# Performance work log

Measured on AMD Instinct MI355X. Metric: run time of the kernel, lower is better.

The kernel has to match this reference:

```python
import jax, jax.numpy as jnp
import numpy as np

# --- constants mirroring init_kwargs ---
DIM = 1024
N_HEADS = 16
N_KV_HEADS = 4
HEAD_DIM = DIM // N_HEADS          # 64
REP = N_HEADS // N_KV_HEADS        # 4
ROPE_THETA = 10000.0
WINDOW = 512
N_GLOBAL = 64
EPS = 1e-6


def setup_inputs() -> dict:
    key = jax.random.key(0)
    ks = jax.random.split(key, 7)
    B, L = 2, 2048
    x = jax.random.normal(ks[0], (B, L, DIM), dtype=jnp.float32)
    s = 0.02
    wq = jax.random.normal(ks[1], (DIM, N_HEADS * HEAD_DIM), dtype=jnp.float32) * s
    wk = jax.random.normal(ks[2], (DIM, N_KV_HEADS * HEAD_DIM), dtype=jnp.float32) * s
    wv = jax.random.normal(ks[3], (DIM, N_KV_HEADS * HEAD_DIM), dtype=jnp.float32) * s
    wo = jax.random.normal(ks[4], (N_HEADS * HEAD_DIM, DIM), dtype=jnp.float32) * s
    gq = jnp.ones((HEAD_DIM,), dtype=jnp.float32) + 0.01 * jax.random.normal(ks[5], (HEAD_DIM,), dtype=jnp.float32)
    gk = jnp.ones((HEAD_DIM,), dtype=jnp.float32) + 0.01 * jax.random.normal(ks[6], (HEAD_DIM,), dtype=jnp.float32)
    return {"x": x, "wq": wq, "wk": wk, "wv": wv, "wo": wo, "gq": gq, "gk": gk}


def _rmsnorm(t, g):
    # QKNorm: RMS norm over head_dim with learnable per-dim scale
    return t * jax.lax.rsqrt(jnp.mean(t * t, axis=-1, keepdims=True) + EPS) * g


def _rope(t, cos, sin):
    # t: [B,H,L,hd]; complex RoPE over consecutive pairs (2i, 2i+1)
    t1 = t[..., 0::2]
    t2 = t[..., 1::2]
    o1 = t1 * cos - t2 * sin
    o2 = t1 * sin + t2 * cos
    return jnp.stack([o1, o2], axis=-1).reshape(t.shape)


def reference(x, wq, wk, wv, wo, gq, gk):
    B, L, D = x.shape
    q = (x @ wq).reshape(B, L, N_HEADS, HEAD_DIM)
    k = (x @ wk).reshape(B, L, N_KV_HEADS, HEAD_DIM)
    v = (x @ wv).reshape(B, L, N_KV_HEADS, HEAD_DIM)
    q = _rmsnorm(q, gq)
    k = _rmsnorm(k, gk)
    q = q.transpose(0, 2, 1, 3)  # [B,H,L,hd]
    k = k.transpose(0, 2, 1, 3)
    v = v.transpose(0, 2, 1, 3)

    # RoPE frequencies (start_pos = 0)
    inv_freq = 1.0 / (ROPE_THETA ** (jnp.arange(0, HEAD_DIM, 2, dtype=jnp.float32) / HEAD_DIM))
    ang = jnp.arange(L, dtype=jnp.float32)[:, None] * inv_freq[None, :]  # [L, hd/2]
    cos, sin = jnp.cos(ang), jnp.sin(ang)
    q = _rope(q, cos, sin)
    k = _rope(k, cos, sin)

    # GQA: repeat kv heads (repeat_interleave on head dim)
    k = jnp.repeat(k, REP, axis=1)
    v = jnp.repeat(v, REP, axis=1)

    scores = jnp.einsum("bhqd,bhkd->bhqk", q, k) / np.sqrt(HEAD_DIM).astype(np.float32)

    # sliding-window + global-token causal mask
    half = WINDOW // 2
    i = jnp.arange(L)[:, None]
    j = jnp.arange(L)[None, :]
    m = (j <= i) & ((j >= i - half) | (j < N_GLOBAL))  # [L,L] bool
    scores = jnp.where(m[None, None], scores, -jnp.inf)

    attn = jax.nn.softmax(scores.astype(jnp.float32), axis=-1).astype(scores.dtype)
    out = jnp.einsum("bhqk,bhkd->bhqd", attn, v)
    out = out.transpose(0, 2, 1, 3).reshape(B, L, N_HEADS * HEAD_DIM)
    return out @ wo
```

## Files before the change

### kernel.cpp

```cpp
#include <hip/hip_runtime.h>
#include <hip/hip_bf16.h>

typedef __bf16 bf16x8 __attribute__((ext_vector_type(8)));
typedef __bf16 bf16x4 __attribute__((ext_vector_type(4)));
typedef float  f32x4  __attribute__((ext_vector_type(4)));
typedef short  s16x4  __attribute__((ext_vector_type(4)));

__device__ __forceinline__ __bf16 to_bf16(float f) {
    __hip_bfloat16 h = __float2bfloat16(f);
    return *reinterpret_cast<__bf16*>(&h);
}

__device__ __forceinline__ f32x4 mfma32(bf16x8 a, bf16x8 b, f32x4 c) {
    return __builtin_amdgcn_mfma_f32_16x16x32_bf16(a, b, c, 0, 0, 0);
}
__device__ __forceinline__ f32x4 mfma16(bf16x4 a, bf16x4 b, f32x4 c) {
#if __has_builtin(__builtin_amdgcn_mfma_f32_16x16x16_bf16)
    return __builtin_amdgcn_mfma_f32_16x16x16_bf16(a, b, c, 0, 0, 0);
#else
    return __builtin_amdgcn_mfma_f32_16x16x16bf16_1k(
        __builtin_bit_cast(s16x4, a), __builtin_bit_cast(s16x4, b), c, 0, 0, 0);
#endif
}

__device__ __forceinline__ void gload_lds16(const __bf16* g, __bf16* l) {
    __builtin_amdgcn_global_load_lds(
        (const __attribute__((address_space(1))) void*)g,
        (__attribute__((address_space(3))) void*)l, 16, 0, 0);
}


__global__ __launch_bounds__(256) void prep_k(const float* __restrict__ wq,
                                              const float* __restrict__ wk,
                                              const float* __restrict__ wv,
                                              const float* __restrict__ x,
                                              __bf16* __restrict__ WqkvT,
                                              __bf16* __restrict__ xb,
                                              float2* __restrict__ rope_tab) {
    int b = blockIdx.x, tid = threadIdx.x;
    if (b >= 3584) {
        int idx = (b - 3584) * 256 + tid;
        int pos = idx >> 5, f = idx & 31;
        float ex = (float)(2 * f) * (1.0f / 64.0f);
        float invf = expf(-ex * 9.210340371976184f);
        float ang = (float)pos * invf;
        rope_tab[idx] = make_float2(cosf(ang), sinf(ang));
        return;
    }
    if (b >= 1536) {
        int i = ((b - 1536) * 256 + tid) * 8;
        f32x4 a = *(const f32x4*)(x + i);
        f32x4 c = *(const f32x4*)(x + i + 4);
        bf16x8 h;
        h[0] = to_bf16(a.x); h[1] = to_bf16(a.y); h[2] = to_bf16(a.z); h[3] = to_bf16(a.w);
        h[4] = to_bf16(c.x); h[5] = to_bf16(c.y); h[6] = to_bf16(c.z); h[7] = to_bf16(c.w);
        *(bf16x8*)(xb + i) = h;
        return;
    }
    __shared__ float tile[32][36];
    const float* src; __bf16* dst; int N, idx;
    if (b < 1024)      { src = wq; dst = WqkvT;                        N = 1024; idx = b; }
    else if (b < 1280) { src = wk; dst = WqkvT + (size_t)1024 * 1024;  N = 256;  idx = b - 1024; }
    else               { src = wv; dst = WqkvT + (size_t)1280 * 1024;  N = 256;  idx = b - 1280; }
    int k0 = (idx & 31) * 32, n0 = (idx >> 5) * 32;
    int row = tid >> 3, c4 = tid & 7;
    *(f32x4*)&tile[row][c4 * 4] = *(const f32x4*)(src + (size_t)(k0 + row) * N + n0 + c4 * 4);
    __syncthreads();
    bf16x4 v;
#pragma unroll
    for (int j = 0; j < 4; ++j) v[j] = to_bf16(tile[c4 * 4 + j][row]);
    *(bf16x4*)&dst[(size_t)(n0 + row) * 1024 + k0 + c4 * 4] = v;
}

#define GEMM_CORE128(A, BT, K, M0, N0)                                          \
    __bf16* smem = (__bf16*)smem_raw;                                           \
    int tid = threadIdx.x;                                                      \
    int m0 = (M0), n0 = (N0);                                                   \
    int wid = tid >> 6, lane = tid & 63;                                        \
    int wm = (wid & 1) * 64, wn = (wid >> 1) * 32;                              \
    int lm = lane & 15, qd = lane >> 4;                                         \
    int srow = tid >> 2, sc4 = tid & 3;                                         \
    f32x4 acc[4][2] = {};                                                       \
    int nt = (K) / 64;                                                          \
    auto STAGE = [&](int bsel, int t) {                                         \
        __bf16* base = smem + bsel * 16384;                                     \
        _Pragma("unroll")                                                       \
        for (int kh = 0; kh < 2; ++kh)                                          \
            gload_lds16((A) + (size_t)(m0 + srow) * (K) + t * 64 + kh * 32 + sc4 * 8, \
                        base + kh * 4096 + wid * 512);                          \
        _Pragma("unroll")                                                       \
        for (int kh = 0; kh < 2; ++kh)                                          \
            gload_lds16((BT) + (size_t)(n0 + srow) * (K) + t * 64 + kh * 32 + sc4 * 8, \
                        base + 8192 + kh * 4096 + wid * 512);                   \
    };                                                                          \
    STAGE(0, 0);                                                                \
    for (int t = 0; t < nt; ++t) {                                              \
        if (t + 1 < nt) {                                                       \
            STAGE((t + 1) & 1, t + 1);                                          \
            asm volatile("s_waitcnt vmcnt(4)" ::: "memory");                    \
        } else {                                                                \
            asm volatile("s_waitcnt vmcnt(0)" ::: "memory");                    \
        }                                                                       \
        __builtin_amdgcn_s_barrier();                                           \
        __builtin_amdgcn_sched_barrier(0);                                      \
        const __bf16* cA = smem + (t & 1) * 16384;                              \
        const __bf16* cB = cA + 8192;                                           \
        _Pragma("unroll")                                                       \
        for (int kh = 0; kh < 2; ++kh) {                                        \
            bf16x8 af[4], bfr[2];                                               \
            _Pragma("unroll")                                                   \
            for (int t4 = 0; t4 < 4; ++t4) {                                    \
                int row = wm + t4 * 16 + lm;                                    \
                af[t4] = *(const bf16x8*)&cA[kh * 4096 + row * 32 + qd * 8];    \
            }                                                                   \
            _Pragma("unroll")                                                   \
            for (int j = 0; j < 2; ++j) {                                       \
                int col = wn + j * 16 + lm;                                     \
                bfr[j] = *(const bf16x8*)&cB[kh * 4096 + col * 32 + qd * 8];    \
            }                                                                   \
            _Pragma("unroll")                                                   \
            for (int ti = 0; ti < 4; ++ti)                                      \
                _Pragma("unroll")                                               \
                for (int tj = 0; tj < 2; ++tj)                                  \
                    acc[ti][tj] = mfma32(af[ti], bfr[tj], acc[ti][tj]);         \
        }                                                                       \
        asm volatile("s_waitcnt lgkmcnt(0)" ::: "memory");                      \
        __builtin_amdgcn_s_barrier();                                           \
    }

__global__ __launch_bounds__(512, 4) void gemmqkv_k(const __bf16* __restrict__ A,
                                                    const __bf16* __restrict__ BT,
                                                    const float2* __restrict__ rope_tab,
                                                    const float* __restrict__ gq,
                                                    const float* __restrict__ gk,
                                                    const float* __restrict__ wo,
                                                    __bf16* __restrict__ Qb,
                                                    __bf16* __restrict__ Kbl,
                                                    __bf16* __restrict__ Vt,
                                                    __bf16* __restrict__ WoT) {
    extern __shared__ char smem_raw[];
    if (blockIdx.y >= 12) {
        float* scr = (float*)smem_raw;
        int bidT = (blockIdx.y - 12) * 32 + blockIdx.x;
        int sub = threadIdx.x >> 8, t8 = threadIdx.x & 255;
        int row = t8 >> 3, c4 = t8 & 7;
        float* my = scr + sub * 1152;
#pragma unroll
        for (int r = 0; r < 4; ++r) {
            int tile = bidT * 8 + r * 2 + sub;
            int k0 = (tile & 31) * 32, n0t = (tile >> 5) * 32;
            __syncthreads();
            *(f32x4*)&my[row * 36 + c4 * 4] =
                *(const f32x4*)(wo + (size_t)(k0 + row) * 1024 + n0t + c4 * 4);
            __syncthreads();
            bf16x4 v;
#pragma unroll
            for (int j = 0; j < 4; ++j) v[j] = to_bf16(my[(c4 * 4 + j) * 36 + row]);
            *(bf16x4*)&WoT[(size_t)(n0t + row) * 1024 + k0 + c4 * 4] = v;
        }
        return;
    }
    __shared__ float ssp[4][128];
    GEMM_CORE128(A, BT, 1024, blockIdx.x * 128, blockIdx.y * 128)
    int head0 = n0 >> 6;
    int quad = wid >> 1;
    int chead = wn & 63;

    if (head0 < 20) {
        int head = head0 + (quad >> 1);
        bool isq = head < 16;
        const float* gvec = isq ? gq : gk;
        float gam[2];
#pragma unroll
        for (int tj = 0; tj < 2; ++tj) gam[tj] = gvec[chead + tj * 16 + lm];

#pragma unroll
        for (int ti = 0; ti < 4; ++ti)
#pragma unroll
            for (int r = 0; r < 4; ++r) {
                float sq = acc[ti][0][r] * acc[ti][0][r] + acc[ti][1][r] * acc[ti][1][r];
                sq += __shfl_xor(sq, 1);
                sq += __shfl_xor(sq, 2);
                sq += __shfl_xor(sq, 4);
                sq += __shfl_xor(sq, 8);
                if (lm == 0) ssp[quad][wm + ti * 16 + qd * 4 + r] = sq;
            }
        __syncthreads();

#pragma unroll
        for (int ti = 0; ti < 4; ++ti)
#pragma unroll
            for (int r = 0; r < 4; ++r) {
                int row = wm + ti * 16 + qd * 4 + r;
                int t = m0 + row;
                int pos = t & 2047, bb = t >> 11;
                float ss = ssp[quad][row] + ssp[quad ^ 1][row];
                float scale = rsqrtf(ss * (1.0f / 64.0f) + 1e-6f);
#pragma unroll
                for (int tj = 0; tj < 2; ++tj) {
                    int cw = chead + tj * 16 + lm;
                    float v = acc[ti][tj][r] * scale * gam[tj];
                    float2 cs = rope_tab[pos * 32 + (cw >> 1)];
                    float pv = __shfl_xor(v, 1);
                    float outv = (cw & 1) ? (pv * cs.y + v * cs.x) : (v * cs.x - pv * cs.y);
                    if (isq) {
                        int kvh = head >> 2, h4 = head & 3;
                        size_t off = (((((size_t)bb * 4 + kvh) * 128 + (pos >> 4)) * 4 + h4) * 16
                                      + (pos & 15)) * 64 + cw;
                        Qb[off] = to_bf16(outv * 0.125f);
                    } else {
                        int kvg = head - 16;
                        Kbl[(((size_t)bb * 4 + kvg) * 2048 + pos) * 64 + cw] = to_bf16(outv);
                    }
                }
            }
    } else {
        __bf16* tvh = smem + (quad >> 1) * 8704;
        int bb = m0 >> 11, pos0 = m0 & 2047;
#pragma unroll
        for (int ti = 0; ti < 4; ++ti)
#pragma unroll
            for (int tj = 0; tj < 2; ++tj)
#pragma unroll
                for (int r = 0; r < 4; ++r) {
                    int row = wm + ti * 16 + qd * 4 + r;
                    int cw = chead + tj * 16 + lm;
                    tvh[cw * 136 + row] = to_bf16(acc[ti][tj][r]);
                }
        __syncthreads();
        int hh = tid >> 8, t8 = tid & 255;
        int kvg = head0 + hh - 20;
        size_t gg = (size_t)bb * 4 + kvg;
        const __bf16* tvr = smem + hh * 8704;
#pragma unroll
        for (int p = 0; p < 4; ++p) {
            int d = p * 16 + (t8 >> 4);
            int tok = (t8 & 15) * 8;
            bf16x8 vvv = *(const bf16x8*)&tvr[d * 136 + tok];
            *(bf16x8*)(Vt + (gg * 64 + d) * 2048 + pos0 + tok) = vvv;
        }
    }
}

__global__ __launch_bounds__(512, 4) void gemm_op_k(const __bf16* __restrict__ A,
                                                    const __bf16* __restrict__ BT,
                                                    float* __restrict__ C) {
    extern __shared__ char smem_raw[];
    __bf16* smem = (__bf16*)smem_raw;
    int tid = threadIdx.x;
    int m0 = blockIdx.x * 128, n0 = blockIdx.y * 64;
    int wid = tid >> 6, lane = tid & 63;
    int wm = (wid & 3) * 32, wn = (wid >> 2) * 32;
    int lm = lane & 15, qd = lane >> 4;
    int srow = tid >> 2, sc4 = tid & 3;
    int bhalf = wid >> 2, bidx = tid & 255;
    int brow = bidx >> 2, bc4 = bidx & 3;
    f32x4 acc[2][2] = {};
    auto STAGE = [&](int bsel, int t) {
        __bf16* base = smem + bsel * 12288;
#pragma unroll
        for (int kh = 0; kh < 2; ++kh)
            gload_lds16(A + (size_t)(m0 + srow) * 1024 + t * 64 + kh * 32 + sc4 * 8,
                        base + kh * 4096 + wid * 512);
        gload_lds16(BT + (size_t)(n0 + brow) * 1024 + t * 64 + bhalf * 32 + bc4 * 8,
                    base + 8192 + bhalf * 2048 + (wid & 3) * 512);
    };
    STAGE(0, 0);
    for (int t = 0; t < 16; ++t) {
        if (t + 1 < 16) {
            STAGE((t + 1) & 1, t + 1);
            asm volatile("s_waitcnt vmcnt(3)" ::: "memory");
        } else {
            asm volatile("s_waitcnt vmcnt(0)" ::: "memory");
        }
        __builtin_amdgcn_s_barrier();
        __builtin_amdgcn_sched_barrier(0);
        const __bf16* cA = smem + (t & 1) * 12288;
        const __bf16* cB = cA + 8192;
#pragma unroll
        for (int kh = 0; kh < 2; ++kh) {
            bf16x8 af[2], bfr[2];
#pragma unroll
            for (int i = 0; i < 2; ++i) {
                int row = wm + i * 16 + lm;
                af[i] = *(const bf16x8*)&cA[kh * 4096 + row * 32 + qd * 8];
                int col = wn + i * 16 + lm;
                bfr[i] = *(const bf16x8*)&cB[kh * 2048 + col * 32 + qd * 8];
            }
#pragma unroll
            for (int ti = 0; ti < 2; ++ti)
#pragma unroll
                for (int tj = 0; tj < 2; ++tj)
                    acc[ti][tj] = mfma32(af[ti], bfr[tj], acc[ti][tj]);
        }
        asm volatile("s_waitcnt lgkmcnt(0)" ::: "memory");
        __builtin_amdgcn_s_barrier();
    }
#pragma unroll
    for (int ti = 0; ti < 2; ++ti)
#pragma unroll
        for (int tj = 0; tj < 2; ++tj)
#pragma unroll
            for (int r = 0; r < 4; ++r) {
                int row = m0 + wm + ti * 16 + qd * 4 + r;
                int col = n0 + wn + tj * 16 + lm;
                C[(size_t)row * 1024 + col] = acc[ti][tj][r];
            }
}

__global__ __launch_bounds__(512, 4) void attn_k(const __bf16* __restrict__ Qb,
                                                 const __bf16* __restrict__ Kbl,
                                                 const __bf16* __restrict__ Vt,
                                                 __bf16* __restrict__ aout) {
    __shared__ __bf16 Kt[2][64 * 64];
    __shared__ __bf16 Vl[2][64 * 64];
    int tid = threadIdx.x, wid = tid >> 6, lane = tid & 63;
    int l15 = lane & 15, quad = lane >> 4;
    int qb = blockIdx.x, kvh = blockIdx.y, b = blockIdx.z;
    int qg = wid >> 2;
    int h4 = wid & 3;
    int iw0 = qb * 32;
    int iw = iw0 + qg * 16;
    int g = b * 4 + kvh;
    int h = kvh * 4 + h4;
    int e7 = l15 & 7;

    int qbi = qb * 2 + qg;
    const __bf16* qp = Qb + ((((size_t)g * 128 + qbi) * 4 + h4) * 16 + l15) * 64 + quad * 8;
    bf16x8 qf0 = *(const bf16x8*)qp;
    bf16x8 qf1 = *(const bf16x8*)(qp + 32);

    int ts = (iw0 - 256) >> 6; if (ts < 1) ts = 1;
    int tmaxb = (iw0 + 31) >> 6;
    int n_all = (tmaxb >= ts) ? (tmaxb - ts + 2) : 1;
    int tmaxw = (iw + 15) >> 6;

    const __bf16* Kg = Kbl + (size_t)g * 2048 * 64;
    const __bf16* Vg = Vt + (size_t)g * 64 * 2048;

    int r0 = tid >> 3, c0 = tid & 7;
    int kl = r0 * 64 + ((c0 ^ (r0 & 7)) * 8);

    bf16x8 kr, vr;
    auto stage_load = [&](int tt) {
        kr = *(const bf16x8*)(Kg + (size_t)tt * 64 * 64 + r0 * 64 + c0 * 8);
        vr = *(const bf16x8*)(Vg + (size_t)r0 * 2048 + tt * 64 + c0 * 8);
    };
    auto stage_write = [&](int buf) {
        *(bf16x8*)&Kt[buf][kl] = kr;
        *(bf16x8*)&Vl[buf][kl] = vr;
    };

    stage_load(0);
    stage_write(0);

    f32x4 o[4] = {};
    float mr = -1e30f, lrp = 0.f;
    int iq = iw + l15;

    for (int idx = 0; idx < n_all; ++idx) {
        int tt = (idx == 0) ? 0 : ts + idx - 1;
        if (idx + 1 < n_all) stage_load(ts + idx);
        __syncthreads();
        int buf = idx & 1;

        f32x4 s[4] = {};
#pragma unroll
        for (int nt = 0; nt < 4; ++nt) {
            const __bf16* kp = &Kt[buf][(nt * 16 + l15) * 64];
            bf16x8 k0 = *(const bf16x8*)(kp + ((quad ^ e7) * 8));
            bf16x8 k1 = *(const bf16x8*)(kp + (((quad + 4) ^ e7) * 8));
            s[nt] = mfma32(k0, qf0, s[nt]);
            s[nt] = mfma32(k1, qf1, s[nt]);
        }

        bool need_mask = (tt >= tmaxw) || (tt >= 1 && tt * 64 < iw + 15 - 256);
        if (need_mask) {
#pragma unroll
            for (int nt = 0; nt < 4; ++nt)
#pragma unroll
                for (int r = 0; r < 4; ++r) {
                    int j = tt * 64 + nt * 16 + quad * 4 + r;
                    bool valid = (j <= iq) && ((j >= iq - 256) || (j < 64));
                    s[nt][r] = valid ? s[nt][r] : -1e30f;
                }
        }

        float mx = -1e30f;
#pragma unroll
        for (int nt = 0; nt < 4; ++nt)
#pragma unroll
            for (int r = 0; r < 4; ++r) mx = fmaxf(mx, s[nt][r]);
        mx = fmaxf(mx, __shfl_xor(mx, 16));
        mx = fmaxf(mx, __shfl_xor(mx, 32));
        float mn = fmaxf(mr, mx);
        float alpha = __expf(mr - mn);
        mr = mn;

        float ps = 0.f;
        bf16x4 pb[4];
#pragma unroll
        for (int nt = 0; nt < 4; ++nt)
#pragma unroll
            for (int r = 0; r < 4; ++r) {
                float pv = __expf(s[nt][r] - mn);
                ps += pv;
                pb[nt][r] = to_bf16(pv);
            }
        lrp = lrp * alpha + ps;

#pragma unroll
        for (int dt = 0; dt < 4; ++dt) {
            o[dt] *= alpha;
            const __bf16* vp = &Vl[buf][(dt * 16 + l15) * 64];
#pragma unroll
            for (int nt = 0; nt < 4; ++nt) {
                int c8 = 2 * nt + (quad >> 1);
                bf16x4 va = *(const bf16x4*)(vp + ((c8 ^ e7) * 8) + (quad & 1) * 4);
                o[dt] = mfma16(va, pb[nt], o[dt]);
            }
        }

        if (idx + 1 < n_all) stage_write((idx + 1) & 1);
    }

    lrp += __shfl_xor(lrp, 16);
    lrp += __shfl_xor(lrp, 32);
    float inv = 1.f / lrp;
    __syncthreads();
    __bf16* pr = (__bf16*)Kt + wid * 16 * 64;
#pragma unroll
    for (int dt = 0; dt < 4; ++dt)
#pragma unroll
        for (int r = 0; r < 4; ++r) {
            int e = dt * 16 + quad * 4 + r;
            int c8 = e >> 3;
            pr[l15 * 64 + ((c8 ^ e7) * 8) + (e & 7)] = to_bf16(o[dt][r] * inv);
        }
    bf16x8 o0 = *(const bf16x8*)(pr + l15 * 64 + (((2 * quad) ^ e7) * 8));
    bf16x8 o1 = *(const bf16x8*)(pr + l15 * 64 + (((2 * quad + 1) ^ e7) * 8));
    __bf16* op = aout + ((size_t)b * 2048 + iw + l15) * 1024 + h * 64 + quad * 16;
    *(bf16x8*)op = o0;
    *(bf16x8*)(op + 8) = o1;
}

extern "C" void kernel_launch(void* const* d_in, const int* in_sizes, int n_in,
                              void* d_out, int out_size, void* d_ws, size_t ws_size,
                              hipStream_t stream) {
    const float* x  = (const float*)d_in[0];
    const float* wq = (const float*)d_in[1];
    const float* wk = (const float*)d_in[2];
    const float* wv = (const float*)d_in[3];
    const float* wo = (const float*)d_in[4];
    const float* gq = (const float*)d_in[5];
    const float* gk = (const float*)d_in[6];
    float* out = (float*)d_out;

    char* ws = (char*)d_ws;
    __bf16*  WqkvT = (__bf16*)ws;
    __bf16*  WoT   = (__bf16*)(ws + 3145728);
    __bf16*  xb_ao = (__bf16*)(ws + 5242880);
    __bf16*  Kbl   = (__bf16*)(ws + 13631488);
    __bf16*  Vt    = (__bf16*)(ws + 15728640);
    __bf16*  Qb    = (__bf16*)(ws + 17825792);
    float2*  rtab  = (float2*)(ws + 26214400);

    prep_k<<<3840, dim3(256), 0, stream>>>(wq, wk, wv, x, WqkvT, xb_ao, rtab);
    gemmqkv_k<<<dim3(32, 16), dim3(512), 65536, stream>>>(xb_ao, WqkvT, rtab, gq, gk, wo,
                                                          Qb, Kbl, Vt, WoT);
    attn_k<<<dim3(64, 4, 2), dim3(512), 0, stream>>>(Qb, Kbl, Vt, xb_ao);
    gemm_op_k<<<dim3(32, 16), dim3(512), 49152, stream>>>(xb_ao, WoT, out);
}
```

Baseline: 143.4 us.

## Fuse x fp32-to-bf16 conversion into QKV GEMM A-tile loading

Drops the separate conversion of x to bf16 in the prep kernel. The QKV GEMM now reads fp32 x straight into registers, converts it to bf16 and writes it to LDS, software-pipelined one tile ahead, while B still uses direct global-to-LDS loads. This removes a full write and re-read of bf16 x and shrinks the prep launch. In exchange, the GEMM reads twice as many bytes for A, and each of the 16 tiles along the x columns is re-read by all 16 column blocks in fp32. It also adds register pressure and VALU conversion work to the main loop.

```diff
diff --git a/kernel.cpp b/kernel.cpp
--- a/kernel.cpp
+++ b/kernel.cpp
@@ -33,28 +33,16 @@
 __global__ __launch_bounds__(256) void prep_k(const float* __restrict__ wq,
                                               const float* __restrict__ wk,
                                               const float* __restrict__ wv,
-                                              const float* __restrict__ x,
                                               __bf16* __restrict__ WqkvT,
-                                              __bf16* __restrict__ xb,
                                               float2* __restrict__ rope_tab) {
     int b = blockIdx.x, tid = threadIdx.x;
-    if (b >= 3584) {
-        int idx = (b - 3584) * 256 + tid;
+    if (b >= 1536) {
+        int idx = (b - 1536) * 256 + tid;
         int pos = idx >> 5, f = idx & 31;
         float ex = (float)(2 * f) * (1.0f / 64.0f);
         float invf = expf(-ex * 9.210340371976184f);
         float ang = (float)pos * invf;
         rope_tab[idx] = make_float2(cosf(ang), sinf(ang));
-        return;
-    }
-    if (b >= 1536) {
-        int i = ((b - 1536) * 256 + tid) * 8;
-        f32x4 a = *(const f32x4*)(x + i);
-        f32x4 c = *(const f32x4*)(x + i + 4);
-        bf16x8 h;
-        h[0] = to_bf16(a.x); h[1] = to_bf16(a.y); h[2] = to_bf16(a.z); h[3] = to_bf16(a.w);
-        h[4] = to_bf16(c.x); h[5] = to_bf16(c.y); h[6] = to_bf16(c.z); h[7] = to_bf16(c.w);
-        *(bf16x8*)(xb + i) = h;
         return;
     }
     __shared__ float tile[32][36];
@@ -72,63 +60,7 @@
     *(bf16x4*)&dst[(size_t)(n0 + row) * 1024 + k0 + c4 * 4] = v;
 }
 
-#define GEMM_CORE128(A, BT, K, M0, N0)                                          \
-    __bf16* smem = (__bf16*)smem_raw;                                           \
-    int tid = threadIdx.x;                                                      \
-    int m0 = (M0), n0 = (N0);                                                   \
-    int wid = tid >> 6, lane = tid & 63;                                        \
-    int wm = (wid & 1) * 64, wn = (wid >> 1) * 32;                              \
-    int lm = lane & 15, qd = lane >> 4;                                         \
-    int srow = tid >> 2, sc4 = tid & 3;                                         \
-    f32x4 acc[4][2] = {};                                                       \
-    int nt = (K) / 64;                                                          \
-    auto STAGE = [&](int bsel, int t) {                                         \
-        __bf16* base = smem + bsel * 16384;                                     \
-        _Pragma("unroll")                                                       \
-        for (int kh = 0; kh < 2; ++kh)                                          \
-            gload_lds16((A) + (size_t)(m0 + srow) * (K) + t * 64 + kh * 32 + sc4 * 8, \
-                        base + kh * 4096 + wid * 512);                          \
-        _Pragma("unroll")                                                       \
-        for (int kh = 0; kh < 2; ++kh)                                          \
-            gload_lds16((BT) + (size_t)(n0 + srow) * (K) + t * 64 + kh * 32 + sc4 * 8, \
-                        base + 8192 + kh * 4096 + wid * 512);                   \
-    };                                                                          \
-    STAGE(0, 0);                                                                \
-    for (int t = 0; t < nt; ++t) {                                              \
-        if (t + 1 < nt) {                                                       \
-            STAGE((t + 1) & 1, t + 1);                                          \
-            asm volatile("s_waitcnt vmcnt(4)" ::: "memory");                    \
-        } else {                                                                \
-            asm volatile("s_waitcnt vmcnt(0)" ::: "memory");                    \
-        }                                                                       \
-        __builtin_amdgcn_s_barrier();                                           \
-        __builtin_amdgcn_sched_barrier(0);                                      \
-        const __bf16* cA = smem + (t & 1) * 16384;                              \
-        const __bf16* cB = cA + 8192;                                           \
-        _Pragma("unroll")                                                       \
-        for (int kh = 0; kh < 2; ++kh) {                                        \
-            bf16x8 af[4], bfr[2];                                               \
-            _Pragma("unroll")                                                   \
-            for (int t4 = 0; t4 < 4; ++t4) {                                    \
-                int row = wm + t4 * 16 + lm;                                    \
-                af[t4] = *(const bf16x8*)&cA[kh * 4096 + row * 32 + qd * 8];    \
-            }                                                                   \
-            _Pragma("unroll")                                                   \
-            for (int j = 0; j < 2; ++j) {                                       \
-                int col = wn + j * 16 + lm;                                     \
-                bfr[j] = *(const bf16x8*)&cB[kh * 4096 + col * 32 + qd * 8];    \
-            }                                                                   \
-            _Pragma("unroll")                                                   \
-            for (int ti = 0; ti < 4; ++ti)                                      \
-                _Pragma("unroll")                                               \
-                for (int tj = 0; tj < 2; ++tj)                                  \
-                    acc[ti][tj] = mfma32(af[ti], bfr[tj], acc[ti][tj]);         \
-        }                                                                       \
-        asm volatile("s_waitcnt lgkmcnt(0)" ::: "memory");                      \
-        __builtin_amdgcn_s_barrier();                                           \
-    }
-
-__global__ __launch_bounds__(512, 4) void gemmqkv_k(const __bf16* __restrict__ A,
+__global__ __launch_bounds__(512, 4) void gemmqkv_k(const float* __restrict__ X,
                                                     const __bf16* __restrict__ BT,
                                                     const float2* __restrict__ rope_tab,
                                                     const float* __restrict__ gq,
@@ -161,7 +93,89 @@
         return;
     }
     __shared__ float ssp[4][128];
-    GEMM_CORE128(A, BT, 1024, blockIdx.x * 128, blockIdx.y * 128)
+    __bf16* smem = (__bf16*)smem_raw;
+    int tid = threadIdx.x;
+    int m0 = blockIdx.x * 128, n0 = blockIdx.y * 128;
+    int wid = tid >> 6, lane = tid & 63;
+    int wm = (wid & 1) * 64, wn = (wid >> 1) * 32;
+    int lm = lane & 15, qd = lane >> 4;
+    int srow = tid >> 2, sc4 = tid & 3;
+    int ac16 = (tid & 3) * 16;
+    int akh = ac16 >> 5, ac4 = (ac16 & 31) >> 3;
+    f32x4 acc[4][2] = {};
+    f32x4 areg[4];
+
+    auto A_LOAD = [&](int t) {
+        const float* ap = X + (size_t)(m0 + srow) * 1024 + t * 64 + ac16;
+        areg[0] = *(const f32x4*)(ap);
+        areg[1] = *(const f32x4*)(ap + 4);
+        areg[2] = *(const f32x4*)(ap + 8);
+        areg[3] = *(const f32x4*)(ap + 12);
+    };
+    auto A_WRITE = [&](int bsel) {
+        __bf16* base = smem + bsel * 16384 + akh * 4096 + srow * 32;
+        bf16x8 w0, w1;
+#pragma unroll
+        for (int j = 0; j < 4; ++j) {
+            w0[j] = to_bf16(areg[0][j]); w0[4 + j] = to_bf16(areg[1][j]);
+            w1[j] = to_bf16(areg[2][j]); w1[4 + j] = to_bf16(areg[3][j]);
+        }
+        *(bf16x8*)&base[ac4 * 8] = w0;
+        *(bf16x8*)&base[(ac4 + 1) * 8] = w1;
+    };
+    auto B_GLOAD = [&](int bsel, int t) {
+        __bf16* base = smem + bsel * 16384 + 8192;
+#pragma unroll
+        for (int kh = 0; kh < 2; ++kh)
+            gload_lds16(BT + (size_t)(n0 + srow) * 1024 + t * 64 + kh * 32 + sc4 * 8,
+                        base + kh * 4096 + wid * 512);
+    };
+
+    A_LOAD(0);
+    B_GLOAD(0, 0);
+    asm volatile("s_waitcnt vmcnt(2)" ::: "memory");
+    A_WRITE(0);
+
+    for (int t = 0; t < 16; ++t) {
+        if (t + 1 < 16) {
+            A_LOAD(t + 1);
+            B_GLOAD((t + 1) & 1, t + 1);
+            asm volatile("s_waitcnt vmcnt(6)" ::: "memory");
+        } else {
+            asm volatile("s_waitcnt vmcnt(0)" ::: "memory");
+        }
+        asm volatile("s_waitcnt lgkmcnt(0)" ::: "memory");
+        __builtin_amdgcn_s_barrier();
+        __builtin_amdgcn_sched_barrier(0);
+        const __bf16* cA = smem + (t & 1) * 16384;
+        const __bf16* cB = cA + 8192;
+#pragma unroll
+        for (int kh = 0; kh < 2; ++kh) {
+            bf16x8 af[4], bfr[2];
+#pragma unroll
+            for (int t4 = 0; t4 < 4; ++t4) {
+                int row = wm + t4 * 16 + lm;
+                af[t4] = *(const bf16x8*)&cA[kh * 4096 + row * 32 + qd * 8];
+            }
+#pragma unroll
+            for (int j = 0; j < 2; ++j) {
+                int col = wn + j * 16 + lm;
+                bfr[j] = *(const bf16x8*)&cB[kh * 4096 + col * 32 + qd * 8];
+            }
+#pragma unroll
+            for (int ti = 0; ti < 4; ++ti)
+#pragma unroll
+                for (int tj = 0; tj < 2; ++tj)
+                    acc[ti][tj] = mfma32(af[ti], bfr[tj], acc[ti][tj]);
+        }
+        if (t + 1 < 16) {
+            asm volatile("s_waitcnt vmcnt(2)" ::: "memory");
+            A_WRITE((t + 1) & 1);
+        }
+        asm volatile("s_waitcnt lgkmcnt(0)" ::: "memory");
+        __builtin_amdgcn_s_barrier();
+    }
+
     int head0 = n0 >> 6;
     int quad = wid >> 1;
     int chead = wn & 63;
@@ -459,15 +473,15 @@
     char* ws = (char*)d_ws;
     __bf16*  WqkvT = (__bf16*)ws;
     __bf16*  WoT   = (__bf16*)(ws + 3145728);
-    __bf16*  xb_ao = (__bf16*)(ws + 5242880);
+    __bf16*  aout  = (__bf16*)(ws + 5242880);
     __bf16*  Kbl   = (__bf16*)(ws + 13631488);
     __bf16*  Vt    = (__bf16*)(ws + 15728640);
     __bf16*  Qb    = (__bf16*)(ws + 17825792);
     float2*  rtab  = (float2*)(ws + 26214400);
 
-    prep_k<<<3840, dim3(256), 0, stream>>>(wq, wk, wv, x, WqkvT, xb_ao, rtab);
-    gemmqkv_k<<<dim3(32, 16), dim3(512), 65536, stream>>>(xb_ao, WqkvT, rtab, gq, gk, wo,
+    prep_k<<<1792, dim3(256), 0, stream>>>(wq, wk, wv, WqkvT, rtab);
+    gemmqkv_k<<<dim3(32, 16), dim3(512), 65536, stream>>>(x, WqkvT, rtab, gq, gk, wo,
                                                           Qb, Kbl, Vt, WoT);
-    attn_k<<<dim3(64, 4, 2), dim3(512), 0, stream>>>(Qb, Kbl, Vt, xb_ao);
-    gemm_op_k<<<dim3(32, 16), dim3(512), 49152, stream>>>(xb_ao, WoT, out);
-}
+    attn_k<<<dim3(64, 4, 2), dim3(512), 0, stream>>>(Qb, Kbl, Vt, aout);
+    gemm_op_k<<<dim3(32, 16), dim3(512), 49152, stream>>>(aout, WoT, out);
+}
```

New measurement: 142.1 us. Within noise of the previous version (-0.9%).
